# Kernel tuning notes

Hardware: AMD Instinct MI355X
Metric: run time of the kernel (lower is better)

## Reference

```python
import jax, jax.numpy as jnp
import numpy as np

N_NODES = 50000
N_EDGES = 800000
IN_DIM = 128
OUT_DIM = 64
NEG_SLOPE = 0.01  # torch F.leaky_relu default


def setup_inputs() -> dict:
    key = jax.random.key(0)
    k1, k2, k3, k4, k5 = jax.random.split(key, 5)
    features = jax.random.normal(k1, (N_NODES, IN_DIM), dtype=jnp.float32)
    # xavier-ish scale for weights
    fc_w = jax.random.normal(k2, (OUT_DIM, IN_DIM), dtype=jnp.float32) * (1.0 / np.sqrt(IN_DIM))
    attn_w = jax.random.normal(k3, (2 * OUT_DIM,), dtype=jnp.float32) * (1.0 / np.sqrt(2 * OUT_DIM))
    src = jax.random.randint(k4, (N_EDGES,), 0, N_NODES, dtype=jnp.int32)
    dst = jax.random.randint(k5, (N_EDGES,), 0, N_NODES, dtype=jnp.int32)
    return {"features": features, "fc_w": fc_w, "attn_w": attn_w, "src": src, "dst": dst}


def reference(features, fc_w, attn_w, src, dst):
    n = features.shape[0]
    out_dim = fc_w.shape[0]
    # z = fc(features), [N, out_dim]
    z = features @ fc_w.T
    # attn_fc([z_src || z_dst]) = z_src @ w_src + z_dst @ w_dst
    a_src = z @ attn_w[:out_dim]   # [N]
    a_dst = z @ attn_w[out_dim:]   # [N]
    e = a_src[src] + a_dst[dst]    # [E] per-edge raw score
    e = jnp.where(e > 0, e, NEG_SLOPE * e)  # leaky_relu
    # edge softmax over incoming edges of each dst node
    e_max = jax.ops.segment_max(e, dst, num_segments=n)      # [N]
    w = jnp.exp(e - e_max[dst])                               # [E]
    denom = jax.ops.segment_sum(w, dst, num_segments=n)       # [N]
    # weighted neighbor sum: sum_e alpha_e * z[src_e]
    num = jax.ops.segment_sum(w[:, None] * z[src], dst, num_segments=n)  # [N, out_dim]
    h = num / jnp.where(denom > 0, denom, 1.0)[:, None]
    # activation = elu
    h = jax.nn.elu(h)
    return h
```

## Files before the change

### kernel.cpp

```cpp
#include <hip/hip_runtime.h>
#include <hip/hip_bf16.h>
#include <hip/hip_fp16.h>

#define N_NODES 50000
#define N_EDGES 800000
#define IN_DIM 128
#define OUT_DIM 64
#define NEG_SLOPE 0.01f
#define NEG_INF (-3.0e38f)

#define N_STRIPS (N_NODES / 16)
#define Z_BLOCKS ((N_STRIPS + 3) / 4)
#define E_I4 (N_EDGES / 4)

#define NB4 ((N_NODES + 31) / 32)
#define CAP4 1024
#define EB 100
#define CHUNK_I4 (E_I4 / EB)

typedef __bf16 bf16x8 __attribute__((ext_vector_type(8)));
typedef float f32x4 __attribute__((ext_vector_type(4)));

__device__ __forceinline__ unsigned short f2bf_us(float f) {
  __hip_bfloat16 h = __float2bfloat16(f);
  return *reinterpret_cast<unsigned short*>(&h);
}
__device__ __forceinline__ bf16x8 pack_bf16(float4 lo, float4 hi) {
  union { bf16x8 v; unsigned short u[8]; } r;
  r.u[0] = f2bf_us(lo.x); r.u[1] = f2bf_us(lo.y);
  r.u[2] = f2bf_us(lo.z); r.u[3] = f2bf_us(lo.w);
  r.u[4] = f2bf_us(hi.x); r.u[5] = f2bf_us(hi.y);
  r.u[6] = f2bf_us(hi.z); r.u[7] = f2bf_us(hi.w);
  return r.v;
}
__device__ __forceinline__ float bflo(unsigned u) {
  return __uint_as_float(u << 16);
}
__device__ __forceinline__ float bfhi(unsigned u) {
  return __uint_as_float(u & 0xffff0000u);
}

__global__ __launch_bounds__(256) void gat_hist(
    const int* __restrict__ dst, int* __restrict__ hist_g) {
  __shared__ int hist[NB4];
  const int tid = threadIdx.x;
  const int bb = blockIdx.x;
  const int i0 = bb * CHUNK_I4;
  for (int i = tid; i < NB4; i += 256) hist[i] = 0;
  __syncthreads();
  for (int t = i0 + tid; t < i0 + CHUNK_I4; t += 256) {
    const int4 d = ((const int4*)dst)[t];
    atomicAdd(&hist[d.x >> 5], 1);
    atomicAdd(&hist[d.y >> 5], 1);
    atomicAdd(&hist[d.z >> 5], 1);
    atomicAdd(&hist[d.w >> 5], 1);
  }
  __syncthreads();
  int* row = hist_g + (size_t)bb * NB4;
  for (int i = tid; i < NB4; i += 256) row[i] = hist[i];
}

__global__ __launch_bounds__(512) void gat_scan(
    const int* __restrict__ hist_g, int* __restrict__ hoff,
    int* __restrict__ cnt) {
  const int nb = blockIdx.x * 512 + threadIdx.x;
  if (nb >= NB4) return;
  int run = 0;
  for (int eb = 0; eb < EB; ++eb) {
    const int v = hist_g[(size_t)eb * NB4 + nb];
    hoff[(size_t)eb * NB4 + nb] = run;
    run += v;
  }
  cnt[nb] = run;
}

__global__ __launch_bounds__(256) void gat_z_scatter(
    const float* __restrict__ feat, const float* __restrict__ fcw,
    const float* __restrict__ attnw, __hip_bfloat16* __restrict__ z,
    float* __restrict__ asrc, float* __restrict__ adst,
    const int* __restrict__ src, const int* __restrict__ dst,
    const int* __restrict__ hoff, unsigned* __restrict__ pairs) {
  if (blockIdx.x >= Z_BLOCKS) {
    __shared__ int cur[NB4];
    const int tid = threadIdx.x;
    const int bb = blockIdx.x - Z_BLOCKS;
    const int i0 = bb * CHUNK_I4;
    const int* hrow = hoff + (size_t)bb * NB4;
    for (int i = tid; i < NB4; i += 256) cur[i] = hrow[i];
    __syncthreads();
    for (int t = i0 + tid; t < i0 + CHUNK_I4; t += 256) {
      const int4 s = ((const int4*)src)[t];
      const int4 d = ((const int4*)dst)[t];
#define BKT_PUT(dd, ss)                                                    \
  {                                                                        \
    const int nb = (dd) >> 5;                                              \
    const int r = atomicAdd(&cur[nb], 1);                                  \
    if (r < CAP4)                                                          \
      pairs[((size_t)nb << 10) + r] =                                      \
          ((unsigned)((dd) & 31) << 16) | (unsigned)(ss);                  \
  }
      BKT_PUT(d.x, s.x)
      BKT_PUT(d.y, s.y)
      BKT_PUT(d.z, s.z)
      BKT_PUT(d.w, s.w)
#undef BKT_PUT
    }
    return;
  }

  const int lane = threadIdx.x & 63;
  const int m = lane & 15;
  const int quad = lane >> 4;
  const int wv = blockIdx.x * 4 + (threadIdx.x >> 6);
  if (wv >= N_STRIPS) return;
  const int n0 = wv * 16;

  bf16x8 bfrag[4][4];
#pragma unroll
  for (int t = 0; t < 4; ++t) {
    const float* wr = fcw + (size_t)(m + 16 * t) * IN_DIM + quad * 8;
#pragma unroll
    for (int c = 0; c < 4; ++c) {
      float4 lo = *(const float4*)(wr + c * 32);
      float4 hi = *(const float4*)(wr + c * 32 + 4);
      bfrag[t][c] = pack_bf16(lo, hi);
    }
  }

  f32x4 acc[4] = {{0.f, 0.f, 0.f, 0.f}, {0.f, 0.f, 0.f, 0.f},
                  {0.f, 0.f, 0.f, 0.f}, {0.f, 0.f, 0.f, 0.f}};
  const float* ar = feat + (size_t)(n0 + m) * IN_DIM + quad * 8;
#pragma unroll
  for (int c = 0; c < 4; ++c) {
    float4 lo = *(const float4*)(ar + c * 32);
    float4 hi = *(const float4*)(ar + c * 32 + 4);
    const bf16x8 af = pack_bf16(lo, hi);
#pragma unroll
    for (int t = 0; t < 4; ++t)
      acc[t] = __builtin_amdgcn_mfma_f32_16x16x32_bf16(af, bfrag[t][c],
                                                       acc[t], 0, 0, 0);
  }

#pragma unroll
  for (int t = 0; t < 4; ++t)
#pragma unroll
    for (int r = 0; r < 4; ++r)
      z[(size_t)(n0 + quad * 4 + r) * OUT_DIM + m + 16 * t] =
          __float2bfloat16(acc[t][r]);

  float aws[4], awd[4];
#pragma unroll
  for (int t = 0; t < 4; ++t) {
    aws[t] = attnw[m + 16 * t];
    awd[t] = attnw[OUT_DIM + m + 16 * t];
  }
  float ps[4], pd[4];
#pragma unroll
  for (int r = 0; r < 4; ++r) {
    float s = 0.f, d = 0.f;
#pragma unroll
    for (int t = 0; t < 4; ++t) {
      s = fmaf(acc[t][r], aws[t], s);
      d = fmaf(acc[t][r], awd[t], d);
    }
    ps[r] = s;
    pd[r] = d;
  }
#pragma unroll
  for (int off = 1; off < 16; off <<= 1) {
#pragma unroll
    for (int r = 0; r < 4; ++r) {
      ps[r] += __shfl_xor(ps[r], off, 64);
      pd[r] += __shfl_xor(pd[r], off, 64);
    }
  }
  if (m == 0) {
#pragma unroll
    for (int r = 0; r < 4; ++r) {
      asrc[n0 + quad * 4 + r] = ps[r];
      adst[n0 + quad * 4 + r] = pd[r];
    }
  }
}

__global__ __launch_bounds__(512) void gat_csr_agg(
    const unsigned* __restrict__ pairs, const int* __restrict__ cnt,
    const __hip_bfloat16* __restrict__ zb, const float* __restrict__ asrc,
    const float* __restrict__ adst, float* __restrict__ out) {
  __shared__ int hist[32];
  __shared__ int noff[33];
  __shared__ int cur[32];
  __shared__ int lsrc[CAP4];
  const int tid = threadIdx.x;
  const int b = blockIdx.x;
  const int c = min(cnt[b], CAP4);
  const unsigned* __restrict__ bp = pairs + ((size_t)b << 10);

  if (tid < 32) hist[tid] = 0;
  __syncthreads();
  for (int i = tid; i < c; i += 512) atomicAdd(&hist[bp[i] >> 16], 1);
  __syncthreads();
  if (tid < 32) {
    const int h = hist[tid];
    int s = h;
#pragma unroll
    for (int off = 1; off < 32; off <<= 1) {
      const int u = __shfl_up(s, off, 64);
      if (tid >= off) s += u;
    }
    noff[tid] = s - h;
    cur[tid] = s - h;
    if (tid == 31) noff[32] = s;
  }
  __syncthreads();
  for (int i = tid; i < c; i += 512) {
    const unsigned p = bp[i];
    const int r = atomicAdd(&cur[p >> 16], 1);
    lsrc[r] = (int)(p & 0xFFFFu);
  }
  __syncthreads();

  const int lane = tid & 63;
  const int wv = tid >> 6;
  const int g = lane >> 4;
  const int sl = lane & 15;
  const int j2 = sl & 3;
  const int eg = sl >> 2;
  const int gbase = lane & 48;

  const int ln = wv * 4 + g;
  const int node = b * 32 + ln;
  if (node >= N_NODES) return;

  const uint4* __restrict__ zp4 = (const uint4*)zb;
  const int o0 = noff[ln];
  const int o1 = noff[ln + 1];
  float4* __restrict__ orow = (float4*)(out + (size_t)node * OUT_DIM);
  if (o0 == o1) {
    if (sl < 4) {
      const float4 zv = {0.f, 0.f, 0.f, 0.f};
#pragma unroll
      for (int v = 0; v < 4; ++v) orow[4 * sl + v] = zv;
    }
    return;
  }
  const float ad = adst[node];

  float m = NEG_INF, dsum = 0.f;
  float acc[16];
#pragma unroll
  for (int cc = 0; cc < 16; ++cc) acc[cc] = 0.f;

  for (int base = o0; base < o1; base += 16) {
    const int cnt2 = min(16, o1 - base);
    int s = 0;
    float ev = NEG_INF;
    if (sl < cnt2) {
      s = lsrc[base + sl];
      const float v = asrc[s] + ad;
      ev = v > 0.f ? v : NEG_SLOPE * v;
    }
    float cm = ev;
#pragma unroll
    for (int off = 1; off < 16; off <<= 1)
      cm = fmaxf(cm, __shfl_xor(cm, off, 64));
    const float nm = fmaxf(m, cm);
    const float scale = __expf(m - nm);
    dsum *= scale;
#pragma unroll
    for (int cc = 0; cc < 16; ++cc) acc[cc] *= scale;
    m = nm;

    const float w = (sl < cnt2) ? __expf(ev - m) : 0.f;
    dsum += w;
    const unsigned pk =
        (unsigned)s |
        ((unsigned)__half_as_ushort(__float2half(w)) << 16);

    const int ngr = (cnt2 + 3) >> 2;
    for (int gg = 0; gg < ngr; ++gg) {
      const unsigned pa = __shfl(pk, gbase + 4 * gg + eg, 64);
      const int sa = (int)(pa & 0xFFFFu);
      const float wa =
          __half2float(__ushort_as_half((unsigned short)(pa >> 16)));
      const uint4 ua = zp4[(size_t)sa * 8 + 2 * j2];
      const uint4 ub = zp4[(size_t)sa * 8 + 2 * j2 + 1];
      acc[0] = fmaf(wa, bflo(ua.x), acc[0]);
      acc[1] = fmaf(wa, bfhi(ua.x), acc[1]);
      acc[2] = fmaf(wa, bflo(ua.y), acc[2]);
      acc[3] = fmaf(wa, bfhi(ua.y), acc[3]);
      acc[4] = fmaf(wa, bflo(ua.z), acc[4]);
      acc[5] = fmaf(wa, bfhi(ua.z), acc[5]);
      acc[6] = fmaf(wa, bflo(ua.w), acc[6]);
      acc[7] = fmaf(wa, bfhi(ua.w), acc[7]);
      acc[8] = fmaf(wa, bflo(ub.x), acc[8]);
      acc[9] = fmaf(wa, bfhi(ub.x), acc[9]);
      acc[10] = fmaf(wa, bflo(ub.y), acc[10]);
      acc[11] = fmaf(wa, bfhi(ub.y), acc[11]);
      acc[12] = fmaf(wa, bflo(ub.z), acc[12]);
      acc[13] = fmaf(wa, bfhi(ub.z), acc[13]);
      acc[14] = fmaf(wa, bflo(ub.w), acc[14]);
      acc[15] = fmaf(wa, bfhi(ub.w), acc[15]);
    }
  }

#pragma unroll
  for (int off = 4; off <= 8; off <<= 1)
#pragma unroll
    for (int cc = 0; cc < 16; ++cc) acc[cc] += __shfl_xor(acc[cc], off, 64);
#pragma unroll
  for (int off = 1; off < 16; off <<= 1) dsum += __shfl_xor(dsum, off, 64);

  if (eg == 0) {
    const float inv = 1.f / (dsum > 0.f ? dsum : 1.f);
#pragma unroll
    for (int v = 0; v < 4; ++v) {
      float4 r;
      float h;
      h = acc[4 * v + 0] * inv; r.x = h > 0.f ? h : expm1f(h);
      h = acc[4 * v + 1] * inv; r.y = h > 0.f ? h : expm1f(h);
      h = acc[4 * v + 2] * inv; r.z = h > 0.f ? h : expm1f(h);
      h = acc[4 * v + 3] * inv; r.w = h > 0.f ? h : expm1f(h);
      orow[4 * j2 + v] = r;
    }
  }
}

extern "C" void kernel_launch(void* const* d_in, const int* in_sizes, int n_in,
                              void* d_out, int out_size, void* d_ws, size_t ws_size,
                              hipStream_t stream) {
  const float* feat  = (const float*)d_in[0];
  const float* fcw   = (const float*)d_in[1];
  const float* attnw = (const float*)d_in[2];
  const int* src     = (const int*)d_in[3];
  const int* dst     = (const int*)d_in[4];
  float* out = (float*)d_out;

  char* ws = (char*)d_ws;
  __hip_bfloat16* z = (__hip_bfloat16*)ws;
  ws += (size_t)N_NODES * OUT_DIM * sizeof(__hip_bfloat16);
  float* asrc = (float*)ws;   ws += (size_t)N_NODES * sizeof(float);
  float* adst = (float*)ws;   ws += (size_t)N_NODES * sizeof(float);
  int* hist_g = (int*)ws;     ws += (size_t)EB * NB4 * sizeof(int);
  int* hoff = (int*)ws;       ws += (size_t)EB * NB4 * sizeof(int);
  int* cnt = (int*)ws;        ws += (size_t)NB4 * sizeof(int);
  unsigned* pairs = (unsigned*)ws;
  ws += (size_t)NB4 * CAP4 * sizeof(unsigned);

  gat_hist<<<EB, 256, 0, stream>>>(dst, hist_g);
  gat_scan<<<(NB4 + 511) / 512, 512, 0, stream>>>(hist_g, hoff, cnt);
  gat_z_scatter<<<Z_BLOCKS + EB, 256, 0, stream>>>(
      feat, fcw, attnw, z, asrc, adst, src, dst, hoff, pairs);
  gat_csr_agg<<<NB4, 512, 0, stream>>>(pairs, cnt, z, asrc, adst, out);
}
```

Measured before the change: 137.9 us.

## Precompute edge exp weights in scatter and drop online softmax max from aggregation

```diff
diff --git a/kernel.cpp b/kernel.cpp
--- a/kernel.cpp
+++ b/kernel.cpp
@@ -7,7 +7,6 @@
 #define IN_DIM 128
 #define OUT_DIM 64
 #define NEG_SLOPE 0.01f
-#define NEG_INF (-3.0e38f)
 
 #define N_STRIPS (N_NODES / 16)
 #define Z_BLOCKS ((N_STRIPS + 3) / 4)
@@ -40,24 +39,104 @@
   return __uint_as_float(u & 0xffff0000u);
 }
 
-__global__ __launch_bounds__(256) void gat_hist(
+__global__ __launch_bounds__(256) void gat_z_hist(
+    const float* __restrict__ feat, const float* __restrict__ fcw,
+    const float* __restrict__ attnw, __hip_bfloat16* __restrict__ z,
+    float* __restrict__ asrc, float* __restrict__ adst,
     const int* __restrict__ dst, int* __restrict__ hist_g) {
-  __shared__ int hist[NB4];
-  const int tid = threadIdx.x;
-  const int bb = blockIdx.x;
-  const int i0 = bb * CHUNK_I4;
-  for (int i = tid; i < NB4; i += 256) hist[i] = 0;
-  __syncthreads();
-  for (int t = i0 + tid; t < i0 + CHUNK_I4; t += 256) {
-    const int4 d = ((const int4*)dst)[t];
-    atomicAdd(&hist[d.x >> 5], 1);
-    atomicAdd(&hist[d.y >> 5], 1);
-    atomicAdd(&hist[d.z >> 5], 1);
-    atomicAdd(&hist[d.w >> 5], 1);
-  }
-  __syncthreads();
-  int* row = hist_g + (size_t)bb * NB4;
-  for (int i = tid; i < NB4; i += 256) row[i] = hist[i];
+  if (blockIdx.x >= Z_BLOCKS) {
+    __shared__ int hist[NB4];
+    const int tid = threadIdx.x;
+    const int bb = blockIdx.x - Z_BLOCKS;
+    const int i0 = bb * CHUNK_I4;
+    for (int i = tid; i < NB4; i += 256) hist[i] = 0;
+    __syncthreads();
+    for (int t = i0 + tid; t < i0 + CHUNK_I4; t += 256) {
+      const int4 d = ((const int4*)dst)[t];
+      atomicAdd(&hist[d.x >> 5], 1);
+      atomicAdd(&hist[d.y >> 5], 1);
+      atomicAdd(&hist[d.z >> 5], 1);
+      atomicAdd(&hist[d.w >> 5], 1);
+    }
+    __syncthreads();
+    int* row = hist_g + (size_t)bb * NB4;
+    for (int i = tid; i < NB4; i += 256) row[i] = hist[i];
+    return;
+  }
+
+  const int lane = threadIdx.x & 63;
+  const int m = lane & 15;
+  const int quad = lane >> 4;
+  const int wv = blockIdx.x * 4 + (threadIdx.x >> 6);
+  if (wv >= N_STRIPS) return;
+  const int n0 = wv * 16;
+
+  bf16x8 bfrag[4][4];
+#pragma unroll
+  for (int t = 0; t < 4; ++t) {
+    const float* wr = fcw + (size_t)(m + 16 * t) * IN_DIM + quad * 8;
+#pragma unroll
+    for (int c = 0; c < 4; ++c) {
+      float4 lo = *(const float4*)(wr + c * 32);
+      float4 hi = *(const float4*)(wr + c * 32 + 4);
+      bfrag[t][c] = pack_bf16(lo, hi);
+    }
+  }
+
+  f32x4 acc[4] = {{0.f, 0.f, 0.f, 0.f}, {0.f, 0.f, 0.f, 0.f},
+                  {0.f, 0.f, 0.f, 0.f}, {0.f, 0.f, 0.f, 0.f}};
+  const float* ar = feat + (size_t)(n0 + m) * IN_DIM + quad * 8;
+#pragma unroll
+  for (int c = 0; c < 4; ++c) {
+    float4 lo = *(const float4*)(ar + c * 32);
+    float4 hi = *(const float4*)(ar + c * 32 + 4);
+    const bf16x8 af = pack_bf16(lo, hi);
+#pragma unroll
+    for (int t = 0; t < 4; ++t)
+      acc[t] = __builtin_amdgcn_mfma_f32_16x16x32_bf16(af, bfrag[t][c],
+                                                       acc[t], 0, 0, 0);
+  }
+
+#pragma unroll
+  for (int t = 0; t < 4; ++t)
+#pragma unroll
+    for (int r = 0; r < 4; ++r)
+      z[(size_t)(n0 + quad * 4 + r) * OUT_DIM + m + 16 * t] =
+          __float2bfloat16(acc[t][r]);
+
+  float aws[4], awd[4];
+#pragma unroll
+  for (int t = 0; t < 4; ++t) {
+    aws[t] = attnw[m + 16 * t];
+    awd[t] = attnw[OUT_DIM + m + 16 * t];
+  }
+  float ps[4], pd[4];
+#pragma unroll
+  for (int r = 0; r < 4; ++r) {
+    float s = 0.f, d = 0.f;
+#pragma unroll
+    for (int t = 0; t < 4; ++t) {
+      s = fmaf(acc[t][r], aws[t], s);
+      d = fmaf(acc[t][r], awd[t], d);
+    }
+    ps[r] = s;
+    pd[r] = d;
+  }
+#pragma unroll
+  for (int off = 1; off < 16; off <<= 1) {
+#pragma unroll
+    for (int r = 0; r < 4; ++r) {
+      ps[r] += __shfl_xor(ps[r], off, 64);
+      pd[r] += __shfl_xor(pd[r], off, 64);
+    }
+  }
+  if (m == 0) {
+#pragma unroll
+    for (int r = 0; r < 4; ++r) {
+      asrc[n0 + quad * 4 + r] = ps[r];
+      adst[n0 + quad * 4 + r] = pd[r];
+    }
+  }
 }
 
 __global__ __launch_bounds__(512) void gat_scan(
@@ -74,131 +153,57 @@
   cnt[nb] = run;
 }
 
-__global__ __launch_bounds__(256) void gat_z_scatter(
-    const float* __restrict__ feat, const float* __restrict__ fcw,
-    const float* __restrict__ attnw, __hip_bfloat16* __restrict__ z,
-    float* __restrict__ asrc, float* __restrict__ adst,
+__global__ __launch_bounds__(1024) void gat_scatter_w(
+    const float* __restrict__ asrc, const float* __restrict__ adst,
     const int* __restrict__ src, const int* __restrict__ dst,
-    const int* __restrict__ hoff, unsigned* __restrict__ pairs) {
-  if (blockIdx.x >= Z_BLOCKS) {
-    __shared__ int cur[NB4];
-    const int tid = threadIdx.x;
-    const int bb = blockIdx.x - Z_BLOCKS;
-    const int i0 = bb * CHUNK_I4;
-    const int* hrow = hoff + (size_t)bb * NB4;
-    for (int i = tid; i < NB4; i += 256) cur[i] = hrow[i];
-    __syncthreads();
-    for (int t = i0 + tid; t < i0 + CHUNK_I4; t += 256) {
-      const int4 s = ((const int4*)src)[t];
-      const int4 d = ((const int4*)dst)[t];
+    const int* __restrict__ hoff, unsigned long long* __restrict__ pairs) {
+  __shared__ int cur[NB4];
+  const int tid = threadIdx.x;
+  const int bb = blockIdx.x;
+  const int i0 = bb * CHUNK_I4;
+  const int* hrow = hoff + (size_t)bb * NB4;
+  for (int i = tid; i < NB4; i += 1024) cur[i] = hrow[i];
+  __syncthreads();
+  for (int t = i0 + tid; t < i0 + CHUNK_I4; t += 1024) {
+    const int4 s = ((const int4*)src)[t];
+    const int4 d = ((const int4*)dst)[t];
 #define BKT_PUT(dd, ss)                                                    \
   {                                                                        \
+    const float a = asrc[ss] + adst[dd];                                   \
+    const float e = a > 0.f ? a : NEG_SLOPE * a;                           \
+    const float w = __expf(e);                                             \
     const int nb = (dd) >> 5;                                              \
     const int r = atomicAdd(&cur[nb], 1);                                  \
     if (r < CAP4)                                                          \
       pairs[((size_t)nb << 10) + r] =                                      \
-          ((unsigned)((dd) & 31) << 16) | (unsigned)(ss);                  \
-  }
-      BKT_PUT(d.x, s.x)
-      BKT_PUT(d.y, s.y)
-      BKT_PUT(d.z, s.z)
-      BKT_PUT(d.w, s.w)
+          ((unsigned long long)__float_as_uint(w) << 32) |                 \
+          (unsigned)((((dd) & 31) << 16) | (ss));                          \
+  }
+    BKT_PUT(d.x, s.x)
+    BKT_PUT(d.y, s.y)
+    BKT_PUT(d.z, s.z)
+    BKT_PUT(d.w, s.w)
 #undef BKT_PUT
-    }
-    return;
-  }
-
-  const int lane = threadIdx.x & 63;
-  const int m = lane & 15;
-  const int quad = lane >> 4;
-  const int wv = blockIdx.x * 4 + (threadIdx.x >> 6);
-  if (wv >= N_STRIPS) return;
-  const int n0 = wv * 16;
-
-  bf16x8 bfrag[4][4];
-#pragma unroll
-  for (int t = 0; t < 4; ++t) {
-    const float* wr = fcw + (size_t)(m + 16 * t) * IN_DIM + quad * 8;
-#pragma unroll
-    for (int c = 0; c < 4; ++c) {
-      float4 lo = *(const float4*)(wr + c * 32);
-      float4 hi = *(const float4*)(wr + c * 32 + 4);
-      bfrag[t][c] = pack_bf16(lo, hi);
-    }
-  }
-
-  f32x4 acc[4] = {{0.f, 0.f, 0.f, 0.f}, {0.f, 0.f, 0.f, 0.f},
-                  {0.f, 0.f, 0.f, 0.f}, {0.f, 0.f, 0.f, 0.f}};
-  const float* ar = feat + (size_t)(n0 + m) * IN_DIM + quad * 8;
-#pragma unroll
-  for (int c = 0; c < 4; ++c) {
-    float4 lo = *(const float4*)(ar + c * 32);
-    float4 hi = *(const float4*)(ar + c * 32 + 4);
-    const bf16x8 af = pack_bf16(lo, hi);
-#pragma unroll
-    for (int t = 0; t < 4; ++t)
-      acc[t] = __builtin_amdgcn_mfma_f32_16x16x32_bf16(af, bfrag[t][c],
-                                                       acc[t], 0, 0, 0);
-  }
-
-#pragma unroll
-  for (int t = 0; t < 4; ++t)
-#pragma unroll
-    for (int r = 0; r < 4; ++r)
-      z[(size_t)(n0 + quad * 4 + r) * OUT_DIM + m + 16 * t] =
-          __float2bfloat16(acc[t][r]);
-
-  float aws[4], awd[4];
-#pragma unroll
-  for (int t = 0; t < 4; ++t) {
-    aws[t] = attnw[m + 16 * t];
-    awd[t] = attnw[OUT_DIM + m + 16 * t];
-  }
-  float ps[4], pd[4];
-#pragma unroll
-  for (int r = 0; r < 4; ++r) {
-    float s = 0.f, d = 0.f;
-#pragma unroll
-    for (int t = 0; t < 4; ++t) {
-      s = fmaf(acc[t][r], aws[t], s);
-      d = fmaf(acc[t][r], awd[t], d);
-    }
-    ps[r] = s;
-    pd[r] = d;
-  }
-#pragma unroll
-  for (int off = 1; off < 16; off <<= 1) {
-#pragma unroll
-    for (int r = 0; r < 4; ++r) {
-      ps[r] += __shfl_xor(ps[r], off, 64);
-      pd[r] += __shfl_xor(pd[r], off, 64);
-    }
-  }
-  if (m == 0) {
-#pragma unroll
-    for (int r = 0; r < 4; ++r) {
-      asrc[n0 + quad * 4 + r] = ps[r];
-      adst[n0 + quad * 4 + r] = pd[r];
-    }
-  }
-}
-
-__global__ __launch_bounds__(512) void gat_csr_agg(
-    const unsigned* __restrict__ pairs, const int* __restrict__ cnt,
-    const __hip_bfloat16* __restrict__ zb, const float* __restrict__ asrc,
-    const float* __restrict__ adst, float* __restrict__ out) {
+  }
+}
+
+__global__ __launch_bounds__(512) void gat_agg(
+    const unsigned long long* __restrict__ pairs, const int* __restrict__ cnt,
+    const __hip_bfloat16* __restrict__ zb, float* __restrict__ out) {
   __shared__ int hist[32];
   __shared__ int noff[33];
   __shared__ int cur[32];
-  __shared__ int lsrc[CAP4];
+  __shared__ float lw[CAP4];
+  __shared__ int ls[CAP4];
   const int tid = threadIdx.x;
   const int b = blockIdx.x;
   const int c = min(cnt[b], CAP4);
-  const unsigned* __restrict__ bp = pairs + ((size_t)b << 10);
+  const unsigned long long* __restrict__ bp = pairs + ((size_t)b << 10);
 
   if (tid < 32) hist[tid] = 0;
   __syncthreads();
-  for (int i = tid; i < c; i += 512) atomicAdd(&hist[bp[i] >> 16], 1);
+  for (int i = tid; i < c; i += 512)
+    atomicAdd(&hist[((const unsigned*)bp)[2 * i] >> 16], 1);
   __syncthreads();
   if (tid < 32) {
     const int h = hist[tid];
@@ -214,9 +219,11 @@
   }
   __syncthreads();
   for (int i = tid; i < c; i += 512) {
-    const unsigned p = bp[i];
-    const int r = atomicAdd(&cur[p >> 16], 1);
-    lsrc[r] = (int)(p & 0xFFFFu);
+    const unsigned long long e = bp[i];
+    const unsigned meta = (unsigned)e;
+    const int r = atomicAdd(&cur[meta >> 16], 1);
+    lw[r] = __uint_as_float((unsigned)(e >> 32));
+    ls[r] = (int)(meta & 0xFFFFu);
   }
   __syncthreads();
 
@@ -226,7 +233,6 @@
   const int sl = lane & 15;
   const int j2 = sl & 3;
   const int eg = sl >> 2;
-  const int gbase = lane & 48;
 
   const int ln = wv * 4 + g;
   const int node = b * 32 + ln;
@@ -235,84 +241,46 @@
   const uint4* __restrict__ zp4 = (const uint4*)zb;
   const int o0 = noff[ln];
   const int o1 = noff[ln + 1];
-  float4* __restrict__ orow = (float4*)(out + (size_t)node * OUT_DIM);
-  if (o0 == o1) {
-    if (sl < 4) {
-      const float4 zv = {0.f, 0.f, 0.f, 0.f};
-#pragma unroll
-      for (int v = 0; v < 4; ++v) orow[4 * sl + v] = zv;
-    }
-    return;
-  }
-  const float ad = adst[node];
-
-  float m = NEG_INF, dsum = 0.f;
+
   float acc[16];
 #pragma unroll
   for (int cc = 0; cc < 16; ++cc) acc[cc] = 0.f;
-
-  for (int base = o0; base < o1; base += 16) {
-    const int cnt2 = min(16, o1 - base);
-    int s = 0;
-    float ev = NEG_INF;
-    if (sl < cnt2) {
-      s = lsrc[base + sl];
-      const float v = asrc[s] + ad;
-      ev = v > 0.f ? v : NEG_SLOPE * v;
-    }
-    float cm = ev;
-#pragma unroll
-    for (int off = 1; off < 16; off <<= 1)
-      cm = fmaxf(cm, __shfl_xor(cm, off, 64));
-    const float nm = fmaxf(m, cm);
-    const float scale = __expf(m - nm);
-    dsum *= scale;
-#pragma unroll
-    for (int cc = 0; cc < 16; ++cc) acc[cc] *= scale;
-    m = nm;
-
-    const float w = (sl < cnt2) ? __expf(ev - m) : 0.f;
+  float dsum = 0.f;
+
+  for (int i = o0 + eg; i < o1; i += 4) {
+    const float w = lw[i];
+    const int s = ls[i];
     dsum += w;
-    const unsigned pk =
-        (unsigned)s |
-        ((unsigned)__half_as_ushort(__float2half(w)) << 16);
-
-    const int ngr = (cnt2 + 3) >> 2;
-    for (int gg = 0; gg < ngr; ++gg) {
-      const unsigned pa = __shfl(pk, gbase + 4 * gg + eg, 64);
-      const int sa = (int)(pa & 0xFFFFu);
-      const float wa =
-          __half2float(__ushort_as_half((unsigned short)(pa >> 16)));
-      const uint4 ua = zp4[(size_t)sa * 8 + 2 * j2];
-      const uint4 ub = zp4[(size_t)sa * 8 + 2 * j2 + 1];
-      acc[0] = fmaf(wa, bflo(ua.x), acc[0]);
-      acc[1] = fmaf(wa, bfhi(ua.x), acc[1]);
-      acc[2] = fmaf(wa, bflo(ua.y), acc[2]);
-      acc[3] = fmaf(wa, bfhi(ua.y), acc[3]);
-      acc[4] = fmaf(wa, bflo(ua.z), acc[4]);
-      acc[5] = fmaf(wa, bfhi(ua.z), acc[5]);
-      acc[6] = fmaf(wa, bflo(ua.w), acc[6]);
-      acc[7] = fmaf(wa, bfhi(ua.w), acc[7]);
-      acc[8] = fmaf(wa, bflo(ub.x), acc[8]);
-      acc[9] = fmaf(wa, bfhi(ub.x), acc[9]);
-      acc[10] = fmaf(wa, bflo(ub.y), acc[10]);
-      acc[11] = fmaf(wa, bfhi(ub.y), acc[11]);
-      acc[12] = fmaf(wa, bflo(ub.z), acc[12]);
-      acc[13] = fmaf(wa, bfhi(ub.z), acc[13]);
-      acc[14] = fmaf(wa, bflo(ub.w), acc[14]);
-      acc[15] = fmaf(wa, bfhi(ub.w), acc[15]);
-    }
-  }
-
-#pragma unroll
-  for (int off = 4; off <= 8; off <<= 1)
+    const uint4 ua = zp4[(size_t)s * 8 + 2 * j2];
+    const uint4 ub = zp4[(size_t)s * 8 + 2 * j2 + 1];
+    acc[0] = fmaf(w, bflo(ua.x), acc[0]);
+    acc[1] = fmaf(w, bfhi(ua.x), acc[1]);
+    acc[2] = fmaf(w, bflo(ua.y), acc[2]);
+    acc[3] = fmaf(w, bfhi(ua.y), acc[3]);
+    acc[4] = fmaf(w, bflo(ua.z), acc[4]);
+    acc[5] = fmaf(w, bfhi(ua.z), acc[5]);
+    acc[6] = fmaf(w, bflo(ua.w), acc[6]);
+    acc[7] = fmaf(w, bfhi(ua.w), acc[7]);
+    acc[8] = fmaf(w, bflo(ub.x), acc[8]);
+    acc[9] = fmaf(w, bfhi(ub.x), acc[9]);
+    acc[10] = fmaf(w, bflo(ub.y), acc[10]);
+    acc[11] = fmaf(w, bfhi(ub.y), acc[11]);
+    acc[12] = fmaf(w, bflo(ub.z), acc[12]);
+    acc[13] = fmaf(w, bfhi(ub.z), acc[13]);
+    acc[14] = fmaf(w, bflo(ub.w), acc[14]);
+    acc[15] = fmaf(w, bfhi(ub.w), acc[15]);
+  }
+
+#pragma unroll
+  for (int off = 4; off <= 8; off <<= 1) {
 #pragma unroll
     for (int cc = 0; cc < 16; ++cc) acc[cc] += __shfl_xor(acc[cc], off, 64);
-#pragma unroll
-  for (int off = 1; off < 16; off <<= 1) dsum += __shfl_xor(dsum, off, 64);
+    dsum += __shfl_xor(dsum, off, 64);
+  }
 
   if (eg == 0) {
     const float inv = 1.f / (dsum > 0.f ? dsum : 1.f);
+    float4* __restrict__ orow = (float4*)(out + (size_t)node * OUT_DIM);
 #pragma unroll
     for (int v = 0; v < 4; ++v) {
       float4 r;
@@ -343,13 +311,13 @@
   float* adst = (float*)ws;   ws += (size_t)N_NODES * sizeof(float);
   int* hist_g = (int*)ws;     ws += (size_t)EB * NB4 * sizeof(int);
   int* hoff = (int*)ws;       ws += (size_t)EB * NB4 * sizeof(int);
-  int* cnt = (int*)ws;        ws += (size_t)NB4 * sizeof(int);
-  unsigned* pairs = (unsigned*)ws;
-  ws += (size_t)NB4 * CAP4 * sizeof(unsigned);
-
-  gat_hist<<<EB, 256, 0, stream>>>(dst, hist_g);
+  int* cnt = (int*)ws;        ws += (size_t)1568 * sizeof(int);
+  unsigned long long* pairs = (unsigned long long*)ws;
+  ws += (size_t)NB4 * CAP4 * sizeof(unsigned long long);
+
+  gat_z_hist<<<Z_BLOCKS + EB, 256, 0, stream>>>(
+      feat, fcw, attnw, z, asrc, adst, dst, hist_g);
   gat_scan<<<(NB4 + 511) / 512, 512, 0, stream>>>(hist_g, hoff, cnt);
-  gat_z_scatter<<<Z_BLOCKS + EB, 256, 0, stream>>>(
-      feat, fcw, attnw, z, asrc, adst, src, dst, hoff, pairs);
-  gat_csr_agg<<<NB4, 512, 0, stream>>>(pairs, cnt, z, asrc, adst, out);
-}
+  gat_scatter_w<<<EB, 1024, 0, stream>>>(asrc, adst, src, dst, hoff, pairs);
+  gat_agg<<<NB4, 512, 0, stream>>>(pairs, cnt, z, out);
+}
```

New measurement: 147.3 us. +6.8%, slower.
